# Optimization experiments

Hardware: AMD Instinct MI355X
Metric: run time of the kernel (lower is better)

Reference implementation:

```python
import jax, jax.numpy as jnp
import numpy as np

WS = 8      # window_size
NH = 4      # num_heads
DM = 128    # d_model
DK = DM // NH


def _rel_pos_index(ws):
    # matches compute_relative_position_index (static, numpy)
    coords = np.stack(np.meshgrid(np.arange(ws), np.arange(ws), indexing='ij'))  # (2,ws,ws)
    cf = coords.reshape(2, -1)                       # (2, ws*ws)
    rel = (cf[:, :, None] - cf[:, None, :]).transpose(1, 2, 0)  # (S,S,2)
    rel[..., 0] += ws - 1
    rel[..., 1] += ws - 1
    rel[..., 0] *= 2 * ws - 1
    return rel.sum(-1)                               # (S,S) int


def _attn_mask(H, W, ws, ss):
    # matches create_attention_mask (static, numpy)
    row = np.broadcast_to(np.arange(H)[:, None], (H, W))
    col = np.broadcast_to(np.arange(W)[None, :], (H, W))
    wid = row // ws * (W // ws) + col // ws
    wid = np.roll(wid, (-ss, -ss), axis=(0, 1))
    wid = wid.reshape(H // ws, ws, W // ws, ws).transpose(0, 2, 1, 3).reshape(-1, ws * ws)
    return (wid[:, :, None] != wid[:, None, :]).astype(np.float32) * -100.0  # (nw,S,S)


def setup_inputs() -> dict:
    key = jax.random.key(0)
    ks = jax.random.split(key, 10)
    B, N = 16, 128 * 128
    w = lambda k, s: jax.random.normal(k, s, jnp.float32) * 0.02
    return {
        "x": jax.random.normal(ks[0], (B, N, DM), jnp.float32),
        "wq": w(ks[1], (DM, DM)), "bq": jnp.zeros((DM,), jnp.float32),
        "wk": w(ks[2], (DM, DM)), "bk": jnp.zeros((DM,), jnp.float32),
        "wv": w(ks[3], (DM, DM)), "bv": jnp.zeros((DM,), jnp.float32),
        "wo": w(ks[4], (DM, DM)), "bo": jnp.zeros((DM,), jnp.float32),
        "bias_table": w(ks[5], ((2 * WS - 1) ** 2, NH)),
        "shift": 1,
    }


def reference(x, wq, bq, wk, bk, wv, bv, wo, bo, bias_table, shift):
    B, N, C = x.shape
    H = W = int(round(N ** 0.5))
    S = WS * WS
    nw_h, nw_w = H // WS, W // WS
    nw = nw_h * nw_w

    # relative position bias: (NH, S, S)
    rel_idx = _rel_pos_index(WS).reshape(-1)
    bias = bias_table[rel_idx].reshape(S, S, NH).transpose(2, 0, 1)

    xi = x.reshape(B, H, W, C)
    if shift:
        xi = jnp.roll(xi, ((-WS) // 2, (-WS) // 2), axis=(1, 2))

    # window partition -> (B*nw, S, C)
    xw = xi.reshape(B, nw_h, WS, nw_w, WS, C).transpose(0, 1, 3, 2, 4, 5).reshape(B * nw, S, C)

    def proj(w_, b_):
        return (xw @ w_ + b_).reshape(B * nw, S, NH, DK).transpose(0, 2, 1, 3)  # (Bn,NH,S,DK)

    q, k, v = proj(wq, bq), proj(wk, bk), proj(wv, bv)

    scores = jnp.einsum('bhnd,bhmd->bhnm', q, k) / jnp.sqrt(jnp.float32(DK))
    if shift:
        mask = jnp.asarray(_attn_mask(H, W, WS, WS // 2))  # (nw,S,S)
        scores = (scores.reshape(B, nw, NH, S, S) + mask[None, :, None]).reshape(B * nw, NH, S, S)
    scores = scores + bias[None]

    attn = jax.nn.softmax(scores, axis=-1)
    out = jnp.einsum('bhnm,bhmd->bhnd', attn, v)          # (Bn,NH,S,DK)
    out = out.transpose(0, 2, 1, 3).reshape(B * nw, S, DM)
    return out @ wo + bo                                   # (B*nw, S, DM)
```

## Files before the change

kernel.cpp:

```cpp
#include <hip/hip_runtime.h>


typedef __attribute__((ext_vector_type(8))) short bf16x8;
typedef __attribute__((ext_vector_type(4))) float f32x4;

#define MFMA16(a, b, c) __builtin_amdgcn_mfma_f32_16x16x32_bf16((a), (b), (c), 0, 0, 0)
#define EXP2F(x) __builtin_amdgcn_exp2f(x)

#define XW_OFF 0
#define STG_OFF 16384
#define LDS_BYTES 32768

__device__ __forceinline__ unsigned int cvt_pk(float lo, float hi) {
  unsigned int r;
  asm("v_cvt_pk_bf16_f32 %0, %1, %2" : "=v"(r) : "v"(lo), "v"(hi));
  return r;
}
__device__ __forceinline__ unsigned short f2bf1(float f) {
  return (unsigned short)(cvt_pk(f, f) & 0xffffu);
}
__device__ __forceinline__ bf16x8 pack8(f32x4 a, f32x4 b) {
  union { unsigned int w[4]; bf16x8 v; } u;
  u.w[0] = cvt_pk(a[0], a[1]); u.w[1] = cvt_pk(a[2], a[3]);
  u.w[2] = cvt_pk(b[0], b[1]); u.w[3] = cvt_pk(b[2], b[3]);
  return u.v;
}
__device__ __forceinline__ bf16x8 packf4(float4 lo, float4 hi) {
  union { unsigned int w[4]; bf16x8 v; } u;
  u.w[0] = cvt_pk(lo.x, lo.y); u.w[1] = cvt_pk(lo.z, lo.w);
  u.w[2] = cvt_pk(hi.x, hi.y); u.w[3] = cvt_pk(hi.z, hi.w);
  return u.v;
}

__global__ void prep_kernel(const float* __restrict__ wq, const float* __restrict__ wk,
                            const float* __restrict__ wv, const float* __restrict__ wo,
                            const float* __restrict__ bias_table,
                            const int* __restrict__ shiftp,
                            unsigned short* __restrict__ wt, float* __restrict__ bias_full) {
  int tid = blockIdx.x * 256 + threadIdx.x;
  int m = tid >> 14, idx = tid & 16383;
  int n = idx >> 7, k = idx & 127;
  const float* w = (m == 0) ? wq : (m == 1) ? wk : (m == 2) ? wv : wo;
  wt[m * 16384 + n * 128 + k] = f2bf1(w[k * 128 + n]);
  if (tid < 16384) {
    int h = tid >> 12, r = tid & 4095;
    int s1 = r >> 6, s2 = r & 63;
    int rel = ((s1 >> 3) - (s2 >> 3) + 7) * 15 + ((s1 & 7) - (s2 & 7) + 7);
    float v = bias_table[rel * 4 + h];
    if (shiftp[0]) {
      int same = (((s1 >> 3) >= 4) == ((s2 >> 3) >= 4)) &
                 (((s1 & 7) >= 4) == ((s2 & 7) >= 4));
      if (!same) v -= 100.0f;
    }
    bias_full[tid] = v * 1.4426950408889634f;
  }
}

__global__ __launch_bounds__(256) void winattn_kernel(
    const float* __restrict__ x,
    const float* __restrict__ bq, const float* __restrict__ bk,
    const float* __restrict__ bv, const float* __restrict__ bo,
    const unsigned short* __restrict__ wt,
    const float* __restrict__ bias_full,
    const int* __restrict__ shiftp,
    float* __restrict__ out) {
  __shared__ __align__(16) char smem[LDS_BYTES];
  const int tid = threadIdx.x;
  const int h = tid >> 6, lane = tid & 63;
  const int g = lane >> 4, c16 = lane & 15;
  const int win = blockIdx.x;
  const int bb = win >> 8, wh = (win >> 4) & 15, ww = win & 15;
  const int ss = shiftp[0] ? 4 : 0;
  const f32x4 z4 = {0.f, 0.f, 0.f, 0.f};

#pragma unroll
  for (int it = 0; it < 4; ++it) {
    int cid = tid + it * 256;
    int s = cid >> 4, cc = (cid & 15) << 3;
    int r0 = (wh * 8 + (s >> 3) + ss) & 127;
    int c0 = (ww * 8 + (s & 7) + ss) & 127;
    const float* src = x + ((bb * 16384 + r0 * 128 + c0) * 128 + cc);
    float4 lo = *(const float4*)src;
    float4 hi = *(const float4*)(src + 4);
    *(bf16x8*)(smem + XW_OFF + s * 256 + ((cc * 2) ^ ((s & 7) << 4))) = packf4(lo, hi);
  }
  __syncthreads();

  bf16x8 qb16[4], kb16[4], vb16[2][2];
  const unsigned short* wq_ = wt + (h * 32 + c16) * 128;
  const unsigned short* wk_ = wt + 16384 + (h * 32 + c16) * 128;
  const unsigned short* wv_ = wt + 32768 + (h * 32 + c16) * 128;

  {
    f32x4 a0[4], a1[4];
#pragma unroll
    for (int t = 0; t < 4; ++t) { a0[t] = z4; a1[t] = z4; }
#pragma unroll
    for (int kk = 0; kk < 4; ++kk) {
      const int co = kk * 32 + g * 8;
      bf16x8 wf0 = *(const bf16x8*)(wk_ + co);
      bf16x8 wf1 = *(const bf16x8*)(wk_ + 2048 + co);
#pragma unroll
      for (int t = 0; t < 4; ++t) {
        int row = t * 16 + c16;
        bf16x8 xf = *(const bf16x8*)(smem + XW_OFF + row * 256 + ((co * 2) ^ ((row & 7) << 4)));
        a0[t] = MFMA16(wf0, xf, a0[t]);
        a1[t] = MFMA16(wf1, xf, a1[t]);
      }
    }
    f32x4 b0 = *(const f32x4*)(bk + h * 32 + g * 4);
    f32x4 b1 = *(const f32x4*)(bk + h * 32 + 16 + g * 4);
#pragma unroll
    for (int t = 0; t < 4; ++t) {
      f32x4 k0, k1;
#pragma unroll
      for (int r = 0; r < 4; ++r) { k0[r] = a0[t][r] + b0[r]; k1[r] = a1[t][r] + b1[r]; }
      kb16[t] = pack8(k0, k1);
    }
  }

  {
    f32x4 a0[4], a1[4];
#pragma unroll
    for (int t = 0; t < 4; ++t) { a0[t] = z4; a1[t] = z4; }
#pragma unroll
    for (int kk = 0; kk < 4; ++kk) {
      const int co = kk * 32 + g * 8;
      bf16x8 wf0 = *(const bf16x8*)(wv_ + co);
      bf16x8 wf1 = *(const bf16x8*)(wv_ + 2048 + co);
#pragma unroll
      for (int t = 0; t < 4; ++t) {
        int row = t * 16 + c16;
        bf16x8 xf = *(const bf16x8*)(smem + XW_OFF + row * 256 + ((co * 2) ^ ((row & 7) << 4)));
        a0[t] = MFMA16(xf, wf0, a0[t]);
        a1[t] = MFMA16(xf, wf1, a1[t]);
      }
    }
    float bv0 = bv[h * 32 + c16];
    float bv1 = bv[h * 32 + 16 + c16];
#pragma unroll
    for (int ks = 0; ks < 2; ++ks) {
      f32x4 v00, v10, v01, v11;
#pragma unroll
      for (int r = 0; r < 4; ++r) {
        v00[r] = a0[2 * ks][r] + bv0;
        v10[r] = a0[2 * ks + 1][r] + bv0;
        v01[r] = a1[2 * ks][r] + bv1;
        v11[r] = a1[2 * ks + 1][r] + bv1;
      }
      vb16[ks][0] = pack8(v00, v10);
      vb16[ks][1] = pack8(v01, v11);
    }
  }

  {
    f32x4 a0[4], a1[4];
#pragma unroll
    for (int t = 0; t < 4; ++t) { a0[t] = z4; a1[t] = z4; }
#pragma unroll
    for (int kk = 0; kk < 4; ++kk) {
      const int co = kk * 32 + g * 8;
      bf16x8 wf0 = *(const bf16x8*)(wq_ + co);
      bf16x8 wf1 = *(const bf16x8*)(wq_ + 2048 + co);
#pragma unroll
      for (int t = 0; t < 4; ++t) {
        int row = t * 16 + c16;
        bf16x8 xf = *(const bf16x8*)(smem + XW_OFF + row * 256 + ((co * 2) ^ ((row & 7) << 4)));
        a0[t] = MFMA16(wf0, xf, a0[t]);
        a1[t] = MFMA16(wf1, xf, a1[t]);
      }
    }
    const float scale = 0.17677669529663687f * 1.4426950408889634f;
    f32x4 b0 = *(const f32x4*)(bq + h * 32 + g * 4);
    f32x4 b1 = *(const f32x4*)(bq + h * 32 + 16 + g * 4);
#pragma unroll
    for (int t = 0; t < 4; ++t) {
      f32x4 q0, q1;
#pragma unroll
      for (int r = 0; r < 4; ++r) {
        q0[r] = (a0[t][r] + b0[r]) * scale;
        q1[r] = (a1[t][r] + b1[r]) * scale;
      }
      qb16[t] = pack8(q0, q1);
    }
  }

  const float* bfh = bias_full + h * 4096 + c16 * 64 + g * 4;
#pragma unroll
  for (int b = 0; b < 4; ++b) {
    f32x4 s0 = MFMA16(kb16[0], qb16[b], z4);
    f32x4 s1 = MFMA16(kb16[1], qb16[b], z4);
    f32x4 s2 = MFMA16(kb16[2], qb16[b], z4);
    f32x4 s3 = MFMA16(kb16[3], qb16[b], z4);
    const float* bfr = bfh + b * 1024;
    f32x4 bia0 = *(const f32x4*)(bfr);
    f32x4 bia1 = *(const f32x4*)(bfr + 16);
    f32x4 bia2 = *(const f32x4*)(bfr + 32);
    f32x4 bia3 = *(const f32x4*)(bfr + 48);
#pragma unroll
    for (int r = 0; r < 4; ++r) {
      s0[r] += bia0[r]; s1[r] += bia1[r]; s2[r] += bia2[r]; s3[r] += bia3[r];
    }
    f32x4 m01, m23;
#pragma unroll
    for (int r = 0; r < 4; ++r) {
      m01[r] = fmaxf(s0[r], s1[r]);
      m23[r] = fmaxf(s2[r], s3[r]);
    }
    float mx = fmaxf(fmaxf(fmaxf(m01[0], m01[1]), fmaxf(m01[2], m01[3])),
                     fmaxf(fmaxf(m23[0], m23[1]), fmaxf(m23[2], m23[3])));
    mx = fmaxf(mx, __shfl_xor(mx, 16));
    mx = fmaxf(mx, __shfl_xor(mx, 32));
#pragma unroll
    for (int r = 0; r < 4; ++r) {
      s0[r] = EXP2F(s0[r] - mx); s1[r] = EXP2F(s1[r] - mx);
      s2[r] = EXP2F(s2[r] - mx); s3[r] = EXP2F(s3[r] - mx);
    }
    f32x4 t01, t23;
#pragma unroll
    for (int r = 0; r < 4; ++r) {
      t01[r] = s0[r] + s1[r];
      t23[r] = s2[r] + s3[r];
    }
    float sum = ((t01[0] + t01[1]) + (t01[2] + t01[3])) +
                ((t23[0] + t23[1]) + (t23[2] + t23[3]));
    sum += __shfl_xor(sum, 16);
    sum += __shfl_xor(sum, 32);
    float inv = 1.0f / sum;
#pragma unroll
    for (int r = 0; r < 4; ++r) {
      s0[r] *= inv; s1[r] *= inv; s2[r] *= inv; s3[r] *= inv;
    }
    bf16x8 pa0 = pack8(s0, s1);
    bf16x8 pa1 = pack8(s2, s3);

    f32x4 o0 = MFMA16(pa0, vb16[0][0], z4);
    f32x4 o1 = MFMA16(pa0, vb16[0][1], z4);
    o0 = MFMA16(pa1, vb16[1][0], o0);
    o1 = MFMA16(pa1, vb16[1][1], o1);

#pragma unroll
    for (int r = 0; r < 4; ++r) {
      int row = b * 16 + g * 4 + r;
      int sw = (row & 7) << 4;
      int col0 = h * 32 + c16;
      *(unsigned short*)(smem + STG_OFF + row * 256 + ((col0 * 2) ^ sw)) = f2bf1(o0[r]);
      *(unsigned short*)(smem + STG_OFF + row * 256 + (((col0 + 16) * 2) ^ sw)) = f2bf1(o1[r]);
    }
  }
  __syncthreads();

  {
    f32x4 acc[8];
#pragma unroll
    for (int nt = 0; nt < 8; ++nt) acc[nt] = z4;
    const int arow = h * 16 + c16;
    const int asw = (arow & 7) << 4;
#pragma unroll
    for (int kk = 0; kk < 4; ++kk) {
      const int co = kk * 32 + g * 8;
      bf16x8 a = *(const bf16x8*)(smem + STG_OFF + arow * 256 + ((co * 2) ^ asw));
#pragma unroll
      for (int nt = 0; nt < 8; ++nt) {
        bf16x8 bfr = *(const bf16x8*)(wt + 49152 + (nt * 16 + c16) * 128 + co);
        acc[nt] = MFMA16(a, bfr, acc[nt]);
      }
    }
#pragma unroll
    for (int nt = 0; nt < 8; ++nt) {
      int n = nt * 16 + c16;
      float bn = bo[n];
#pragma unroll
      for (int r = 0; r < 4; ++r) {
        int row = h * 16 + g * 4 + r;
        out[(size_t)win * 8192 + (size_t)(row * 128 + n)] = acc[nt][r] + bn;
      }
    }
  }
}

extern "C" void kernel_launch(void* const* d_in, const int* in_sizes, int n_in,
                              void* d_out, int out_size, void* d_ws, size_t ws_size,
                              hipStream_t stream) {
  const float* x = (const float*)d_in[0];
  const float* wq = (const float*)d_in[1];
  const float* bq = (const float*)d_in[2];
  const float* wk = (const float*)d_in[3];
  const float* bk = (const float*)d_in[4];
  const float* wv = (const float*)d_in[5];
  const float* bv = (const float*)d_in[6];
  const float* wo = (const float*)d_in[7];
  const float* bo = (const float*)d_in[8];
  const float* bias_table = (const float*)d_in[9];
  const int* shiftp = (const int*)d_in[10];

  unsigned short* wt = (unsigned short*)d_ws;
  float* bias_full = (float*)((char*)d_ws + 131072);

  prep_kernel<<<256, 256, 0, stream>>>(wq, wk, wv, wo, bias_table, shiftp, wt, bias_full);
  winattn_kernel<<<4096, 256, 0, stream>>>(x, bq, bk, bv, bo, wt, bias_full, shiftp,
                                           (float*)d_out);
}
```

Before: 161.7 us.

## Fuse QKV projections into one k-loop, halve LDS, add MFMA priority hints

Merges the three separate Q, K and V projection loops into a single loop that loads each x fragment from LDS once and feeds all six MFMA chains. It adds a barrier and reuses the same LDS region for the attention-output staging buffer, cutting LDS per block from 32KB to 16KB so more blocks can be resident. It also wraps the MFMA sections in s_setprio hints. The cost is more live accumulator registers (24 f32x4 at once), which may raise VGPR pressure and limit occupancy, plus one extra barrier.

Result: slower. 168.3 us (+4.1%).

```diff
diff --git a/kernel.cpp b/kernel.cpp
--- a/kernel.cpp
+++ b/kernel.cpp
@@ -6,10 +6,10 @@
 
 #define MFMA16(a, b, c) __builtin_amdgcn_mfma_f32_16x16x32_bf16((a), (b), (c), 0, 0, 0)
 #define EXP2F(x) __builtin_amdgcn_exp2f(x)
-
-#define XW_OFF 0
-#define STG_OFF 16384
-#define LDS_BYTES 32768
+#define PRIO1() __builtin_amdgcn_s_setprio(1)
+#define PRIO0() __builtin_amdgcn_s_setprio(0)
+
+#define LDS_BYTES 16384
 
 __device__ __forceinline__ unsigned int cvt_pk(float lo, float hi) {
   unsigned int r;
@@ -82,59 +82,69 @@
     const float* src = x + ((bb * 16384 + r0 * 128 + c0) * 128 + cc);
     float4 lo = *(const float4*)src;
     float4 hi = *(const float4*)(src + 4);
-    *(bf16x8*)(smem + XW_OFF + s * 256 + ((cc * 2) ^ ((s & 7) << 4))) = packf4(lo, hi);
+    *(bf16x8*)(smem + s * 256 + ((cc * 2) ^ ((s & 7) << 4))) = packf4(lo, hi);
   }
   __syncthreads();
 
-  bf16x8 qb16[4], kb16[4], vb16[2][2];
+  f32x4 qacc[2][4], kacc[2][4], vacc[4][2];
+#pragma unroll
+  for (int i = 0; i < 4; ++i) {
+    qacc[0][i] = z4; qacc[1][i] = z4;
+    kacc[0][i] = z4; kacc[1][i] = z4;
+    vacc[i][0] = z4; vacc[i][1] = z4;
+  }
   const unsigned short* wq_ = wt + (h * 32 + c16) * 128;
   const unsigned short* wk_ = wt + 16384 + (h * 32 + c16) * 128;
   const unsigned short* wv_ = wt + 32768 + (h * 32 + c16) * 128;
-
+  PRIO1();
+#pragma unroll
+  for (int kk = 0; kk < 4; ++kk) {
+    const int co = kk * 32 + g * 8;
+    bf16x8 xfr[4];
+#pragma unroll
+    for (int t = 0; t < 4; ++t) {
+      int row = t * 16 + c16;
+      xfr[t] = *(const bf16x8*)(smem + row * 256 + ((co * 2) ^ ((row & 7) << 4)));
+    }
+    bf16x8 wqf0 = *(const bf16x8*)(wq_ + co);
+    bf16x8 wqf1 = *(const bf16x8*)(wq_ + 2048 + co);
+    bf16x8 wkf0 = *(const bf16x8*)(wk_ + co);
+    bf16x8 wkf1 = *(const bf16x8*)(wk_ + 2048 + co);
+    bf16x8 wvf0 = *(const bf16x8*)(wv_ + co);
+    bf16x8 wvf1 = *(const bf16x8*)(wv_ + 2048 + co);
+#pragma unroll
+    for (int t = 0; t < 4; ++t) {
+      qacc[0][t] = MFMA16(wqf0, xfr[t], qacc[0][t]);
+      qacc[1][t] = MFMA16(wqf1, xfr[t], qacc[1][t]);
+      kacc[0][t] = MFMA16(wkf0, xfr[t], kacc[0][t]);
+      kacc[1][t] = MFMA16(wkf1, xfr[t], kacc[1][t]);
+      vacc[t][0] = MFMA16(xfr[t], wvf0, vacc[t][0]);
+      vacc[t][1] = MFMA16(xfr[t], wvf1, vacc[t][1]);
+    }
+  }
+  PRIO0();
+  __syncthreads();
+
+  bf16x8 qb16[4], kb16[4], vb16[2][2];
   {
-    f32x4 a0[4], a1[4];
-#pragma unroll
-    for (int t = 0; t < 4; ++t) { a0[t] = z4; a1[t] = z4; }
-#pragma unroll
-    for (int kk = 0; kk < 4; ++kk) {
-      const int co = kk * 32 + g * 8;
-      bf16x8 wf0 = *(const bf16x8*)(wk_ + co);
-      bf16x8 wf1 = *(const bf16x8*)(wk_ + 2048 + co);
-#pragma unroll
-      for (int t = 0; t < 4; ++t) {
-        int row = t * 16 + c16;
-        bf16x8 xf = *(const bf16x8*)(smem + XW_OFF + row * 256 + ((co * 2) ^ ((row & 7) << 4)));
-        a0[t] = MFMA16(wf0, xf, a0[t]);
-        a1[t] = MFMA16(wf1, xf, a1[t]);
-      }
-    }
-    f32x4 b0 = *(const f32x4*)(bk + h * 32 + g * 4);
-    f32x4 b1 = *(const f32x4*)(bk + h * 32 + 16 + g * 4);
+    const float scale = 0.17677669529663687f * 1.4426950408889634f;
+    f32x4 bq4[2], bk4[2];
+    bq4[0] = *(const f32x4*)(bq + h * 32 + g * 4);
+    bq4[1] = *(const f32x4*)(bq + h * 32 + 16 + g * 4);
+    bk4[0] = *(const f32x4*)(bk + h * 32 + g * 4);
+    bk4[1] = *(const f32x4*)(bk + h * 32 + 16 + g * 4);
 #pragma unroll
     for (int t = 0; t < 4; ++t) {
-      f32x4 k0, k1;
-#pragma unroll
-      for (int r = 0; r < 4; ++r) { k0[r] = a0[t][r] + b0[r]; k1[r] = a1[t][r] + b1[r]; }
+      f32x4 q0, q1, k0, k1;
+#pragma unroll
+      for (int r = 0; r < 4; ++r) {
+        q0[r] = (qacc[0][t][r] + bq4[0][r]) * scale;
+        q1[r] = (qacc[1][t][r] + bq4[1][r]) * scale;
+        k0[r] = kacc[0][t][r] + bk4[0][r];
+        k1[r] = kacc[1][t][r] + bk4[1][r];
+      }
+      qb16[t] = pack8(q0, q1);
       kb16[t] = pack8(k0, k1);
-    }
-  }
-
-  {
-    f32x4 a0[4], a1[4];
-#pragma unroll
-    for (int t = 0; t < 4; ++t) { a0[t] = z4; a1[t] = z4; }
-#pragma unroll
-    for (int kk = 0; kk < 4; ++kk) {
-      const int co = kk * 32 + g * 8;
-      bf16x8 wf0 = *(const bf16x8*)(wv_ + co);
-      bf16x8 wf1 = *(const bf16x8*)(wv_ + 2048 + co);
-#pragma unroll
-      for (int t = 0; t < 4; ++t) {
-        int row = t * 16 + c16;
-        bf16x8 xf = *(const bf16x8*)(smem + XW_OFF + row * 256 + ((co * 2) ^ ((row & 7) << 4)));
-        a0[t] = MFMA16(xf, wf0, a0[t]);
-        a1[t] = MFMA16(xf, wf1, a1[t]);
-      }
     }
     float bv0 = bv[h * 32 + c16];
     float bv1 = bv[h * 32 + 16 + c16];
@@ -143,55 +153,25 @@
       f32x4 v00, v10, v01, v11;
 #pragma unroll
       for (int r = 0; r < 4; ++r) {
-        v00[r] = a0[2 * ks][r] + bv0;
-        v10[r] = a0[2 * ks + 1][r] + bv0;
-        v01[r] = a1[2 * ks][r] + bv1;
-        v11[r] = a1[2 * ks + 1][r] + bv1;
+        v00[r] = vacc[2 * ks][0][r] + bv0;
+        v10[r] = vacc[2 * ks + 1][0][r] + bv0;
+        v01[r] = vacc[2 * ks][1][r] + bv1;
+        v11[r] = vacc[2 * ks + 1][1][r] + bv1;
       }
       vb16[ks][0] = pack8(v00, v10);
       vb16[ks][1] = pack8(v01, v11);
     }
   }
 
-  {
-    f32x4 a0[4], a1[4];
-#pragma unroll
-    for (int t = 0; t < 4; ++t) { a0[t] = z4; a1[t] = z4; }
-#pragma unroll
-    for (int kk = 0; kk < 4; ++kk) {
-      const int co = kk * 32 + g * 8;
-      bf16x8 wf0 = *(const bf16x8*)(wq_ + co);
-      bf16x8 wf1 = *(const bf16x8*)(wq_ + 2048 + co);
-#pragma unroll
-      for (int t = 0; t < 4; ++t) {
-        int row = t * 16 + c16;
-        bf16x8 xf = *(const bf16x8*)(smem + XW_OFF + row * 256 + ((co * 2) ^ ((row & 7) << 4)));
-        a0[t] = MFMA16(wf0, xf, a0[t]);
-        a1[t] = MFMA16(wf1, xf, a1[t]);
-      }
-    }
-    const float scale = 0.17677669529663687f * 1.4426950408889634f;
-    f32x4 b0 = *(const f32x4*)(bq + h * 32 + g * 4);
-    f32x4 b1 = *(const f32x4*)(bq + h * 32 + 16 + g * 4);
-#pragma unroll
-    for (int t = 0; t < 4; ++t) {
-      f32x4 q0, q1;
-#pragma unroll
-      for (int r = 0; r < 4; ++r) {
-        q0[r] = (a0[t][r] + b0[r]) * scale;
-        q1[r] = (a1[t][r] + b1[r]) * scale;
-      }
-      qb16[t] = pack8(q0, q1);
-    }
-  }
-
   const float* bfh = bias_full + h * 4096 + c16 * 64 + g * 4;
 #pragma unroll
   for (int b = 0; b < 4; ++b) {
+    PRIO1();
     f32x4 s0 = MFMA16(kb16[0], qb16[b], z4);
     f32x4 s1 = MFMA16(kb16[1], qb16[b], z4);
     f32x4 s2 = MFMA16(kb16[2], qb16[b], z4);
     f32x4 s3 = MFMA16(kb16[3], qb16[b], z4);
+    PRIO0();
     const float* bfr = bfh + b * 1024;
     f32x4 bia0 = *(const f32x4*)(bfr);
     f32x4 bia1 = *(const f32x4*)(bfr + 16);
@@ -234,18 +214,20 @@
     bf16x8 pa0 = pack8(s0, s1);
     bf16x8 pa1 = pack8(s2, s3);
 
+    PRIO1();
     f32x4 o0 = MFMA16(pa0, vb16[0][0], z4);
     f32x4 o1 = MFMA16(pa0, vb16[0][1], z4);
     o0 = MFMA16(pa1, vb16[1][0], o0);
     o1 = MFMA16(pa1, vb16[1][1], o1);
+    PRIO0();
 
 #pragma unroll
     for (int r = 0; r < 4; ++r) {
       int row = b * 16 + g * 4 + r;
       int sw = (row & 7) << 4;
       int col0 = h * 32 + c16;
-      *(unsigned short*)(smem + STG_OFF + row * 256 + ((col0 * 2) ^ sw)) = f2bf1(o0[r]);
-      *(unsigned short*)(smem + STG_OFF + row * 256 + (((col0 + 16) * 2) ^ sw)) = f2bf1(o1[r]);
+      *(unsigned short*)(smem + row * 256 + ((col0 * 2) ^ sw)) = f2bf1(o0[r]);
+      *(unsigned short*)(smem + row * 256 + (((col0 + 16) * 2) ^ sw)) = f2bf1(o1[r]);
     }
   }
   __syncthreads();
@@ -256,16 +238,18 @@
     for (int nt = 0; nt < 8; ++nt) acc[nt] = z4;
     const int arow = h * 16 + c16;
     const int asw = (arow & 7) << 4;
+    PRIO1();
 #pragma unroll
     for (int kk = 0; kk < 4; ++kk) {
       const int co = kk * 32 + g * 8;
-      bf16x8 a = *(const bf16x8*)(smem + STG_OFF + arow * 256 + ((co * 2) ^ asw));
+      bf16x8 a = *(const bf16x8*)(smem + arow * 256 + ((co * 2) ^ asw));
 #pragma unroll
       for (int nt = 0; nt < 8; ++nt) {
         bf16x8 bfr = *(const bf16x8*)(wt + 49152 + (nt * 16 + c16) * 128 + co);
         acc[nt] = MFMA16(a, bfr, acc[nt]);
       }
     }
+    PRIO0();
 #pragma unroll
     for (int nt = 0; nt < 8; ++nt) {
       int n = nt * 16 + c16;
```
